# Kernel tuning notes

Measured on AMD Instinct MI355X. Metric: run time of the kernel, lower is better.

## Reference

```python
import jax, jax.numpy as jnp
import numpy as np

NX = NY = NZ = 64          # grid.shape
SPACING = 0.5              # Angstrom grid spacing
RESOLUTION = 2.0           # map resolution cutoff (A)
N_ATOMS = 128
K = 6                      # _range = 6 Gaussian terms (em=False)
CHUNK = 65536              # chunk_size over grid points


def setup_inputs() -> dict:
    key = jax.random.key(0)
    k1, k2, k3 = jax.random.split(key, 3)
    box = jnp.array([NX * SPACING, NY * SPACING, NZ * SPACING], jnp.float32)
    # atom coordinates uniform inside the box
    X = jax.random.uniform(k1, (N_ATOMS, 3), jnp.float32) * box
    # aw > 0, bw < 0 as produced by _setup_coeffs (aw = a*(-bw/pi)^1.5, bw = -pi^2/b)
    aw = jax.random.uniform(k2, (N_ATOMS, K), jnp.float32) * 4.0 + 0.5
    bw = -(jax.random.uniform(k3, (N_ATOMS, K), jnp.float32) * 4.0 + 0.5)
    # real-space grid, origin at 0 (center_shift folded in)
    xs = jnp.arange(NX, dtype=jnp.float32) * SPACING
    ys = jnp.arange(NY, dtype=jnp.float32) * SPACING
    zs = jnp.arange(NZ, dtype=jnp.float32) * SPACING
    gx, gy, gz = jnp.meshgrid(xs, ys, zs, indexing='ij')
    real_grid_flat = jnp.stack([gx, gy, gz], axis=-1).reshape(-1, 3)  # (G,3)
    # Fourier frequency magnitudes and radial Hamming filter (set_filter_and_mask)
    fx = jnp.fft.fftshift(jnp.fft.fftfreq(NX, SPACING)).astype(jnp.float32)
    fy = jnp.fft.fftshift(jnp.fft.fftfreq(NY, SPACING)).astype(jnp.float32)
    fz = jnp.fft.fftshift(jnp.fft.fftfreq(NZ, SPACING)).astype(jnp.float32)
    fxx, fyy, fzz = jnp.meshgrid(fx, fy, fz, indexing='ij')
    f_mag = jnp.sqrt(fxx ** 2 + fyy ** 2 + fzz ** 2)
    cutoff = 1.0 / RESOLUTION
    r_scaled = f_mag / cutoff
    hamming = jnp.where(f_mag <= cutoff,
                        0.54 + 0.46 * jnp.cos(jnp.pi * r_scaled),
                        0.0).astype(jnp.float32)
    return {"X": X, "aw": aw, "bw": bw,
            "real_grid_flat": real_grid_flat, "hamming": hamming}


def _density_flat(real_grid_flat, X, aw, bw):
    """Chunked sum-of-Gaussians splatting: density[g] = sum_a sum_k aw[a,k]*exp(bw[a,k]*|g-x_a|^2)."""
    def chunk_density(grid_chunk):  # (C,3)
        # squared distances grid-chunk x atoms, (C, A); cdist(...,p=2)**2 == sum of squared diffs
        d2 = jnp.sum((grid_chunk[:, None, :] - X[None, :, :]) ** 2, axis=-1)
        dens = jnp.zeros((grid_chunk.shape[0],), dtype=grid_chunk.dtype)
        for k in range(K):  # fixed small K=6, avoids (C,A,K) materialization
            dens = dens + jnp.sum(aw[None, :, k] * jnp.exp(bw[None, :, k] * d2), axis=-1)
        return dens
    G = real_grid_flat.shape[0]
    chunks = real_grid_flat.reshape(G // CHUNK, CHUNK, 3)
    dens = jax.lax.map(chunk_density, chunks)  # (n_chunks, CHUNK)
    return dens.reshape(G)


def _to_f_density(rho):
    ax = (-3, -2, -1)
    return jnp.fft.fftshift(
        jnp.fft.fftn(jnp.fft.ifftshift(rho, axes=ax), axes=ax, norm='ortho'), axes=ax)


def _to_density(f_map):
    ax = (-3, -2, -1)
    return jnp.fft.fftshift(
        jnp.fft.ifftn(jnp.fft.ifftshift(f_map, axes=ax), axes=ax, norm='ortho'), axes=ax)


def reference(X, aw, bw, real_grid_flat, hamming):
    rho = _density_flat(real_grid_flat, X, aw, bw).reshape(NX, NY, NZ)
    f_rho = _to_f_density(rho)
    f_filtered = f_rho * hamming            # radial Hamming low-pass at 1/resolution
    out = _to_density(f_filtered).real      # filtered real-space density
    # normalize() helper: zero mean, unit (population) std
    return (out - out.mean()) / (out.std() + 1e-8)
```

## Files before the change

kernel.cpp:

```cpp
#include <hip/hip_runtime.h>
#include <math.h>

#define NG (64*64*64)

typedef __bf16 v8bf __attribute__((ext_vector_type(8)));
typedef float  v4f  __attribute__((ext_vector_type(4)));

#define WS_W    0
#define WS_PART (2*1024*1024)

#define K_LIVE(k) ((k) <= 16 || (k) >= 48)

__device__ __forceinline__ float2 cadd(float2 a, float2 b) {
    return make_float2(a.x + b.x, a.y + b.y);
}
__device__ __forceinline__ float2 csub(float2 a, float2 b) {
    return make_float2(a.x - b.x, a.y - b.y);
}
template <bool CONJ>
__device__ __forceinline__ float2 mulmi(float2 a) {
    return CONJ ? make_float2(-a.y, a.x) : make_float2(a.y, -a.x);
}

template <bool CONJ>
__device__ __forceinline__ void fft8(const float2 x[8], float2 y[8])
{
    const float r = 0.70710678118654752f;
    float2 ee0 = cadd(x[0], x[4]), ee1 = csub(x[0], x[4]);
    float2 eo0 = cadd(x[2], x[6]), eo1 = csub(x[2], x[6]);
    float2 E0 = cadd(ee0, eo0), E2 = csub(ee0, eo0);
    float2 me = mulmi<CONJ>(eo1);
    float2 E1 = cadd(ee1, me), E3 = csub(ee1, me);
    float2 oe0 = cadd(x[1], x[5]), oe1 = csub(x[1], x[5]);
    float2 oo0 = cadd(x[3], x[7]), oo1 = csub(x[3], x[7]);
    float2 O0 = cadd(oe0, oo0), O2 = csub(oe0, oo0);
    float2 mo = mulmi<CONJ>(oo1);
    float2 O1 = cadd(oe1, mo), O3 = csub(oe1, mo);
    float2 W1O1 = CONJ ? make_float2(r * (O1.x - O1.y), r * (O1.x + O1.y))
                       : make_float2(r * (O1.x + O1.y), r * (O1.y - O1.x));
    float2 W2O2 = mulmi<CONJ>(O2);
    float2 W3O3 = CONJ ? make_float2(-r * (O3.x + O3.y), r * (O3.x - O3.y))
                       : make_float2(r * (O3.y - O3.x), -r * (O3.x + O3.y));
    y[0] = cadd(E0, O0);   y[4] = csub(E0, O0);
    y[1] = cadd(E1, W1O1); y[5] = csub(E1, W1O1);
    y[2] = cadd(E2, W2O2); y[6] = csub(E2, W2O2);
    y[3] = cadd(E3, W3O3); y[7] = csub(E3, W3O3);
}

template <bool CONJ>
__device__ __forceinline__ void xf64(const float2 xin[8], float2* L, int es,
                                     int t, const float2* tw, float2 y[8],
                                     bool active)
{
    float2 b[8];
    if (active) {
        fft8<CONJ>(xin, b);
#pragma unroll
        for (int k1 = 0; k1 < 8; ++k1) {
            float2 wv = tw[(t * k1) & 63];
            float ws = CONJ ? -wv.y : wv.y;
            float tr = b[k1].x * wv.x - b[k1].y * ws;
            float ti = b[k1].x * ws + b[k1].y * wv.x;
            b[k1] = make_float2(tr, ti);
        }
#pragma unroll
        for (int k1 = 0; k1 < 8; ++k1)
            L[(k1 * 8 + t) * es] = b[k1];
    }
    __syncthreads();
    if (active) {
        float2 a[8];
#pragma unroll
        for (int n1 = 0; n1 < 8; ++n1) a[n1] = L[(t * 8 + n1) * es];
        fft8<CONJ>(a, y);
    }
}

__device__ __forceinline__ void make_tw(float2* tw, int tid)
{
    if (tid < 64) {
        float ang = -6.28318530717958647692f * (float)tid / 64.0f;
        float s, c;
        sincosf(ang, &s, &c);
        tw[tid] = make_float2(c, s);
    }
}

__global__ __launch_bounds__(512) void density_fftz_kernel(
    const float* __restrict__ X, const float* __restrict__ aw,
    const float* __restrict__ bw, float2* __restrict__ W2)
{
    __shared__ __align__(16) __bf16 Ah[16][776];
    __shared__ __align__(16) __bf16 Al[16][776];
    __shared__ float2 D[16][66];
    __shared__ float2 tw[64];

    int tid = threadIdx.x;
    make_tw(tw, tid);

    int blk = blockIdx.x;
    int x  = blk >> 2;
    int yq = blk & 3;
    float px = 0.5f * (float)x;

    {
        int row = tid >> 5;
        int a0  = (tid & 31) * 4;
        float py = 0.5f * (float)(yq * 16 + row);
#pragma unroll
        for (int ai = 0; ai < 4; ++ai) {
            int a = a0 + ai;
            float dxa = px - X[3 * a + 0];
            float dya = py - X[3 * a + 1];
            float d2 = dxa * dxa + dya * dya;
            int jb = a * 6;
#pragma unroll
            for (int p = 0; p < 3; ++p) {
                int j = jb + 2 * p;
                float e0 = aw[j] * __expf(bw[j] * d2);
                float e1 = aw[j + 1] * __expf(bw[j + 1] * d2);
                __bf16 h0 = (__bf16)e0, h1 = (__bf16)e1;
                __bf16 l0 = (__bf16)(e0 - (float)h0);
                __bf16 l1 = (__bf16)(e1 - (float)h1);
                unsigned hp = ((unsigned)__builtin_bit_cast(unsigned short, h1) << 16)
                            | (unsigned)__builtin_bit_cast(unsigned short, h0);
                unsigned lp = ((unsigned)__builtin_bit_cast(unsigned short, l1) << 16)
                            | (unsigned)__builtin_bit_cast(unsigned short, l0);
                *(unsigned*)&Ah[row][j] = hp;
                *(unsigned*)&Al[row][j] = lp;
            }
        }
    }
    __syncthreads();

    {
        int w = tid >> 6;
        int l = tid & 63;
        int m = l & 15;
        int g = l >> 4;
        int zt = w & 3;
        int kh = w >> 2;
        float pz = 0.5f * (float)(zt * 16 + m);
        int jb0 = kh * 384 + g * 8;
        v4f accHH = {0.f, 0.f, 0.f, 0.f};
        v4f accHL = {0.f, 0.f, 0.f, 0.f};
        v4f accLH = {0.f, 0.f, 0.f, 0.f};
        const __bf16* ahp = &Ah[m][jb0];
        const __bf16* alp = &Al[m][jb0];
#pragma unroll 2
        for (int ks = 0; ks < 12; ++ks) {
            v8bf aH = *(const v8bf*)(ahp + ks * 32);
            v8bf aL = *(const v8bf*)(alp + ks * 32);
            v8bf bH, bL;
#pragma unroll
            for (int p = 0; p < 4; ++p) {
                int j = jb0 + ks * 32 + 2 * p;
                float2 bwp = *(const float2*)(bw + j);
                int a0 = j / 6, a1 = (j + 1) / 6;
                float dz0 = pz - X[3 * a0 + 2];
                float dz1 = pz - X[3 * a1 + 2];
                float e0 = __expf(bwp.x * dz0 * dz0);
                float e1 = __expf(bwp.y * dz1 * dz1);
                __bf16 h0 = (__bf16)e0, h1 = (__bf16)e1;
                bH[2 * p]     = h0;
                bH[2 * p + 1] = h1;
                bL[2 * p]     = (__bf16)(e0 - (float)h0);
                bL[2 * p + 1] = (__bf16)(e1 - (float)h1);
            }
            accHH = __builtin_amdgcn_mfma_f32_16x16x32_bf16(aH, bH, accHH, 0, 0, 0);
            accHL = __builtin_amdgcn_mfma_f32_16x16x32_bf16(aH, bL, accHL, 0, 0, 0);
            accLH = __builtin_amdgcn_mfma_f32_16x16x32_bf16(aL, bH, accLH, 0, 0, 0);
        }
#pragma unroll
        for (int r = 0; r < 4; ++r) {
            float s = accHH[r] + accHL[r] + accLH[r];
            if (kh == 0) D[g * 4 + r][zt * 16 + m].x = s;
            else         D[g * 4 + r][zt * 16 + m].y = s;
        }
    }
    __syncthreads();

    bool active = tid < 128;
    int lid = (tid >> 3) & 15, t = tid & 7;
    float2 xin[8], y[8];
    if (active) {
#pragma unroll
        for (int n2 = 0; n2 < 8; ++n2) {
            float2 v = D[lid][8 * n2 + t];
            xin[n2] = make_float2(v.x + v.y, 0.f);
        }
    }
    xf64<false>(xin, &D[lid][0], 1, t, tw, y, active);
    if (active) {
        int ybase = yq * 16 + lid;
#pragma unroll
        for (int k2 = 0; k2 < 8; ++k2) {
            int kz = t + 8 * k2;
            if (K_LIVE(kz))
                W2[kz * 4096 + x * 64 + ybase] = y[k2];
        }
    }
}

__global__ __launch_bounds__(512) void plane_kernel(
    float2* __restrict__ W2, const float* __restrict__ ham,
    double* __restrict__ partial)
{
    __shared__ float2 P[64][66];
    __shared__ float2 tw[64];
    __shared__ double red[8];
    int tid = threadIdx.x;
    make_tw(tw, tid);

    int z0 = blockIdx.x <= 16 ? blockIdx.x : blockIdx.x + 31;
    const float4* src = (const float4*)(W2 + z0 * 4096);
#pragma unroll
    for (int q = 0; q < 4; ++q) {
        int i = tid + q * 512;
        float4 v = src[i];
        int e = i * 2;
        P[e >> 6][e & 63] = make_float2(v.x, v.y);
        P[e >> 6][(e & 63) + 1] = make_float2(v.z, v.w);
    }
    __syncthreads();

    int lid = tid >> 3, t = tid & 7;
    float2 xin[8], y[8];

#pragma unroll
    for (int n2 = 0; n2 < 8; ++n2) xin[n2] = P[lid][8 * n2 + t];
    xf64<false>(xin, &P[lid][0], 1, t, tw, y, true);
    __syncthreads();
#pragma unroll
    for (int k2 = 0; k2 < 8; ++k2) P[lid][t + 8 * k2] = y[k2];
    __syncthreads();

    bool kyLive = K_LIVE(lid);
#pragma unroll
    for (int n2 = 0; n2 < 8; ++n2) xin[n2] = P[8 * n2 + t][lid];
    xf64<false>(xin, &P[0][lid], 66, t, tw, y, kyLive);
    if (kyLive) {
        int hyz = ((lid + 32) & 63) * 64 + ((z0 + 32) & 63);
#pragma unroll
        for (int k2 = 0; k2 < 8; ++k2) {
            int kx = t + 8 * k2;
            float h = ham[((kx + 32) & 63) * 4096 + hyz];
            y[k2].x *= h; y[k2].y *= h;
        }
    }
    {
        double s2 = 0.0;
        if (kyLive) {
#pragma unroll
            for (int k2 = 0; k2 < 8; ++k2)
                s2 += (double)y[k2].x * y[k2].x + (double)y[k2].y * y[k2].y;
        }
#pragma unroll
        for (int off = 32; off > 0; off >>= 1)
            s2 += __shfl_down(s2, off, 64);
        if ((tid & 63) == 0) red[tid >> 6] = s2;
        if (z0 == 0 && tid == 0)
            partial[64] = (double)y[0].x;
    }
    __syncthreads();
#pragma unroll
    for (int k2 = 0; k2 < 8; ++k2)
        P[t + 8 * k2][lid] = kyLive ? y[k2] : make_float2(0.f, 0.f);
    __syncthreads();
    if (tid == 0) {
        double s = 0.0;
#pragma unroll
        for (int i = 0; i < 8; ++i) s += red[i];
        partial[z0] = s;
    }

#pragma unroll
    for (int n2 = 0; n2 < 8; ++n2) xin[n2] = P[8 * n2 + t][lid];
    xf64<true>(xin, &P[0][lid], 66, t, tw, y, kyLive);
    __syncthreads();
    if (kyLive) {
#pragma unroll
        for (int k2 = 0; k2 < 8; ++k2) P[t + 8 * k2][lid] = y[k2];
    }
    __syncthreads();

#pragma unroll
    for (int n2 = 0; n2 < 8; ++n2) xin[n2] = P[lid][8 * n2 + t];
    xf64<true>(xin, &P[lid][0], 1, t, tw, y, true);
#pragma unroll
    for (int k2 = 0; k2 < 8; ++k2)
        W2[z0 * 4096 + lid * 64 + t + 8 * k2] = y[k2];
}

__global__ __launch_bounds__(128) void invz_norm_kernel(
    const float2* __restrict__ W2, const double* __restrict__ partial,
    float* __restrict__ outr)
{
    __shared__ float2 ln[16][66];
    __shared__ float2 tw[64];
    __shared__ float nrm[2];
    int tid = threadIdx.x;
    make_tw(tw, tid);
    if (tid < 64) {
        double s = K_LIVE(tid) ? partial[tid] : 0.0;
#pragma unroll
        for (int off = 32; off > 0; off >>= 1)
            s += __shfl_down(s, off, 64);
        if (tid == 0) {
            double mean = partial[64] * (1.0 / 262144.0);
            double var = s * (1.0 / 262144.0 / 262144.0) - mean * mean;
            nrm[0] = (float)mean;
            nrm[1] = (float)(1.0 / (sqrt(var > 0.0 ? var : 0.0) + 1e-8));
        }
    }
    __syncthreads();

    int lid = tid >> 3, t = tid & 7;
    int L = blockIdx.x * 16 + lid;
    float2 xin[8], y[8];
#pragma unroll
    for (int n2 = 0; n2 < 8; ++n2) {
        int kz = 8 * n2 + t;
        xin[n2] = K_LIVE(kz) ? W2[kz * 4096 + L] : make_float2(0.f, 0.f);
    }
    xf64<true>(xin, &ln[lid][0], 1, t, tw, y, true);

    float mean = nrm[0], rstd = nrm[1];
#pragma unroll
    for (int k2 = 0; k2 < 8; ++k2) {
        float v = y[k2].x * (1.0f / 262144.0f);
        outr[L * 64 + t + 8 * k2] = (v - mean) * rstd;
    }
}

extern "C" void kernel_launch(void* const* d_in, const int* in_sizes, int n_in,
                              void* d_out, int out_size, void* d_ws,
                              size_t ws_size, hipStream_t stream)
{
    const float* X   = (const float*)d_in[0];
    const float* aw  = (const float*)d_in[1];
    const float* bw  = (const float*)d_in[2];
    const float* ham = (const float*)d_in[4];
    float* out = (float*)d_out;

    char* ws = (char*)d_ws;
    float2* W2   = (float2*)(ws + WS_W);
    double* part = (double*)(ws + WS_PART);

    density_fftz_kernel<<<256, 512, 0, stream>>>(X, aw, bw, W2);
    plane_kernel<<<33, 512, 0, stream>>>(W2, ham, part);
    invz_norm_kernel<<<256, 128, 0, stream>>>(W2, part, out);
}
```

Measured before the change: 24.87 us.

## Exploit Hermitian symmetry in kz and fuse plane and inverse-z kernels

Because the density is real, its spectrum is Hermitian, so only kz 0..16 are computed and stored. The mirrored planes are rebuilt from their conjugates in the final inverse-z pass, and the energy sum is doubled for the non-zero planes. The plane kernel and the inverse-z/normalize kernel are merged into one launch: 17 producer blocks process the planes, and 64 consumer blocks spin on a global atomic counter before running the last pass. This removes one kernel launch and about half the plane work, but it relies on all producer blocks being scheduled alongside the spinning consumers, and it adds a spin-wait latency.

```diff
diff --git a/kernel.cpp b/kernel.cpp
--- a/kernel.cpp
+++ b/kernel.cpp
@@ -8,6 +8,7 @@
 
 #define WS_W    0
 #define WS_PART (2*1024*1024)
+#define WS_FLAG (WS_PART + 256)
 
 #define K_LIVE(k) ((k) <= 16 || (k) >= 48)
 
@@ -88,7 +89,8 @@
 
 __global__ __launch_bounds__(512) void density_fftz_kernel(
     const float* __restrict__ X, const float* __restrict__ aw,
-    const float* __restrict__ bw, float2* __restrict__ W2)
+    const float* __restrict__ bw, float2* __restrict__ W2,
+    int* __restrict__ flag)
 {
     __shared__ __align__(16) __bf16 Ah[16][776];
     __shared__ __align__(16) __bf16 Al[16][776];
@@ -97,6 +99,8 @@
 
     int tid = threadIdx.x;
     make_tw(tw, tid);
+    if (blockIdx.x == 0 && tid == 0)
+        __hip_atomic_store(flag, 0, __ATOMIC_RELAXED, __HIP_MEMORY_SCOPE_AGENT);
 
     int blk = blockIdx.x;
     int x  = blk >> 2;
@@ -196,140 +200,154 @@
 #pragma unroll
         for (int k2 = 0; k2 < 8; ++k2) {
             int kz = t + 8 * k2;
-            if (K_LIVE(kz))
+            if (kz <= 16)
                 W2[kz * 4096 + x * 64 + ybase] = y[k2];
         }
     }
 }
 
-__global__ __launch_bounds__(512) void plane_kernel(
+__global__ __launch_bounds__(512) void spectrum_inv_kernel(
     float2* __restrict__ W2, const float* __restrict__ ham,
-    double* __restrict__ partial)
+    double* __restrict__ partial, float* __restrict__ outr,
+    int* __restrict__ flag)
 {
     __shared__ float2 P[64][66];
     __shared__ float2 tw[64];
     __shared__ double red[8];
+    __shared__ float nrm[2];
+
     int tid = threadIdx.x;
+    int bid = blockIdx.x;
     make_tw(tw, tid);
 
-    int z0 = blockIdx.x <= 16 ? blockIdx.x : blockIdx.x + 31;
-    const float4* src = (const float4*)(W2 + z0 * 4096);
-#pragma unroll
-    for (int q = 0; q < 4; ++q) {
-        int i = tid + q * 512;
-        float4 v = src[i];
-        int e = i * 2;
-        P[e >> 6][e & 63] = make_float2(v.x, v.y);
-        P[e >> 6][(e & 63) + 1] = make_float2(v.z, v.w);
-    }
-    __syncthreads();
-
-    int lid = tid >> 3, t = tid & 7;
-    float2 xin[8], y[8];
-
-#pragma unroll
-    for (int n2 = 0; n2 < 8; ++n2) xin[n2] = P[lid][8 * n2 + t];
-    xf64<false>(xin, &P[lid][0], 1, t, tw, y, true);
-    __syncthreads();
-#pragma unroll
-    for (int k2 = 0; k2 < 8; ++k2) P[lid][t + 8 * k2] = y[k2];
-    __syncthreads();
-
-    bool kyLive = K_LIVE(lid);
-#pragma unroll
-    for (int n2 = 0; n2 < 8; ++n2) xin[n2] = P[8 * n2 + t][lid];
-    xf64<false>(xin, &P[0][lid], 66, t, tw, y, kyLive);
-    if (kyLive) {
-        int hyz = ((lid + 32) & 63) * 64 + ((z0 + 32) & 63);
+    if (bid < 17) {
+        int z0 = bid;
+        const float4* src = (const float4*)(W2 + z0 * 4096);
+#pragma unroll
+        for (int q = 0; q < 4; ++q) {
+            int i = tid + q * 512;
+            float4 v = src[i];
+            int e = i * 2;
+            P[e >> 6][e & 63] = make_float2(v.x, v.y);
+            P[e >> 6][(e & 63) + 1] = make_float2(v.z, v.w);
+        }
+        __syncthreads();
+
+        int lid = tid >> 3, t = tid & 7;
+        float2 xin[8], y[8];
+
+#pragma unroll
+        for (int n2 = 0; n2 < 8; ++n2) xin[n2] = P[lid][8 * n2 + t];
+        xf64<false>(xin, &P[lid][0], 1, t, tw, y, true);
+        __syncthreads();
+#pragma unroll
+        for (int k2 = 0; k2 < 8; ++k2) P[lid][t + 8 * k2] = y[k2];
+        __syncthreads();
+
+        bool kyLive = K_LIVE(lid);
+#pragma unroll
+        for (int n2 = 0; n2 < 8; ++n2) xin[n2] = P[8 * n2 + t][lid];
+        xf64<false>(xin, &P[0][lid], 66, t, tw, y, kyLive);
+        if (kyLive) {
+            int hyz = ((lid + 32) & 63) * 64 + ((z0 + 32) & 63);
+#pragma unroll
+            for (int k2 = 0; k2 < 8; ++k2) {
+                int kx = t + 8 * k2;
+                float h = ham[((kx + 32) & 63) * 4096 + hyz];
+                y[k2].x *= h; y[k2].y *= h;
+            }
+        }
+        {
+            double s2 = 0.0;
+            if (kyLive) {
+#pragma unroll
+                for (int k2 = 0; k2 < 8; ++k2)
+                    s2 += (double)y[k2].x * y[k2].x + (double)y[k2].y * y[k2].y;
+            }
+#pragma unroll
+            for (int off = 32; off > 0; off >>= 1)
+                s2 += __shfl_down(s2, off, 64);
+            if ((tid & 63) == 0) red[tid >> 6] = s2;
+            if (z0 == 0 && tid == 0)
+                partial[17] = (double)y[0].x;
+        }
+        __syncthreads();
+#pragma unroll
+        for (int k2 = 0; k2 < 8; ++k2)
+            P[t + 8 * k2][lid] = kyLive ? y[k2] : make_float2(0.f, 0.f);
+        __syncthreads();
+        if (tid == 0) {
+            double s = 0.0;
+#pragma unroll
+            for (int i = 0; i < 8; ++i) s += red[i];
+            partial[z0] = (z0 == 0 ? 1.0 : 2.0) * s;
+        }
+
+#pragma unroll
+        for (int n2 = 0; n2 < 8; ++n2) xin[n2] = P[8 * n2 + t][lid];
+        xf64<true>(xin, &P[0][lid], 66, t, tw, y, kyLive);
+        __syncthreads();
+        if (kyLive) {
+#pragma unroll
+            for (int k2 = 0; k2 < 8; ++k2) P[t + 8 * k2][lid] = y[k2];
+        }
+        __syncthreads();
+
+#pragma unroll
+        for (int n2 = 0; n2 < 8; ++n2) xin[n2] = P[lid][8 * n2 + t];
+        xf64<true>(xin, &P[lid][0], 1, t, tw, y, true);
+#pragma unroll
+        for (int k2 = 0; k2 < 8; ++k2)
+            W2[z0 * 4096 + lid * 64 + t + 8 * k2] = y[k2];
+
+        __syncthreads();
+        if (tid == 0)
+            __hip_atomic_fetch_add(flag, 1, __ATOMIC_ACQ_REL,
+                                   __HIP_MEMORY_SCOPE_AGENT);
+    } else {
+        if (tid == 0) {
+            while (__hip_atomic_load(flag, __ATOMIC_ACQUIRE,
+                                     __HIP_MEMORY_SCOPE_AGENT) < 17)
+                __builtin_amdgcn_s_sleep(8);
+        }
+        __syncthreads();
+
+        if (tid < 64) {
+            double s = (tid <= 16) ? partial[tid] : 0.0;
+#pragma unroll
+            for (int off = 32; off > 0; off >>= 1)
+                s += __shfl_down(s, off, 64);
+            if (tid == 0) {
+                double mean = partial[17] * (1.0 / 262144.0);
+                double var = s * (1.0 / 262144.0 / 262144.0) - mean * mean;
+                nrm[0] = (float)mean;
+                nrm[1] = (float)(1.0 / (sqrt(var > 0.0 ? var : 0.0) + 1e-8));
+            }
+        }
+
+        int lid = tid >> 3, t = tid & 7;
+        int L = (bid - 17) * 64 + lid;
+        float2 xin[8], y[8];
+#pragma unroll
+        for (int n2 = 0; n2 < 8; ++n2) {
+            int kz = 8 * n2 + t;
+            if (kz <= 16) {
+                xin[n2] = W2[kz * 4096 + L];
+            } else if (kz >= 48) {
+                float2 v = W2[(64 - kz) * 4096 + L];
+                xin[n2] = make_float2(v.x, -v.y);
+            } else {
+                xin[n2] = make_float2(0.f, 0.f);
+            }
+        }
+        xf64<true>(xin, &P[lid][0], 1, t, tw, y, true);
+
+        float mean = nrm[0], rstd = nrm[1];
 #pragma unroll
         for (int k2 = 0; k2 < 8; ++k2) {
-            int kx = t + 8 * k2;
-            float h = ham[((kx + 32) & 63) * 4096 + hyz];
-            y[k2].x *= h; y[k2].y *= h;
-        }
-    }
-    {
-        double s2 = 0.0;
-        if (kyLive) {
-#pragma unroll
-            for (int k2 = 0; k2 < 8; ++k2)
-                s2 += (double)y[k2].x * y[k2].x + (double)y[k2].y * y[k2].y;
-        }
-#pragma unroll
-        for (int off = 32; off > 0; off >>= 1)
-            s2 += __shfl_down(s2, off, 64);
-        if ((tid & 63) == 0) red[tid >> 6] = s2;
-        if (z0 == 0 && tid == 0)
-            partial[64] = (double)y[0].x;
-    }
-    __syncthreads();
-#pragma unroll
-    for (int k2 = 0; k2 < 8; ++k2)
-        P[t + 8 * k2][lid] = kyLive ? y[k2] : make_float2(0.f, 0.f);
-    __syncthreads();
-    if (tid == 0) {
-        double s = 0.0;
-#pragma unroll
-        for (int i = 0; i < 8; ++i) s += red[i];
-        partial[z0] = s;
-    }
-
-#pragma unroll
-    for (int n2 = 0; n2 < 8; ++n2) xin[n2] = P[8 * n2 + t][lid];
-    xf64<true>(xin, &P[0][lid], 66, t, tw, y, kyLive);
-    __syncthreads();
-    if (kyLive) {
-#pragma unroll
-        for (int k2 = 0; k2 < 8; ++k2) P[t + 8 * k2][lid] = y[k2];
-    }
-    __syncthreads();
-
-#pragma unroll
-    for (int n2 = 0; n2 < 8; ++n2) xin[n2] = P[lid][8 * n2 + t];
-    xf64<true>(xin, &P[lid][0], 1, t, tw, y, true);
-#pragma unroll
-    for (int k2 = 0; k2 < 8; ++k2)
-        W2[z0 * 4096 + lid * 64 + t + 8 * k2] = y[k2];
-}
-
-__global__ __launch_bounds__(128) void invz_norm_kernel(
-    const float2* __restrict__ W2, const double* __restrict__ partial,
-    float* __restrict__ outr)
-{
-    __shared__ float2 ln[16][66];
-    __shared__ float2 tw[64];
-    __shared__ float nrm[2];
-    int tid = threadIdx.x;
-    make_tw(tw, tid);
-    if (tid < 64) {
-        double s = K_LIVE(tid) ? partial[tid] : 0.0;
-#pragma unroll
-        for (int off = 32; off > 0; off >>= 1)
-            s += __shfl_down(s, off, 64);
-        if (tid == 0) {
-            double mean = partial[64] * (1.0 / 262144.0);
-            double var = s * (1.0 / 262144.0 / 262144.0) - mean * mean;
-            nrm[0] = (float)mean;
-            nrm[1] = (float)(1.0 / (sqrt(var > 0.0 ? var : 0.0) + 1e-8));
-        }
-    }
-    __syncthreads();
-
-    int lid = tid >> 3, t = tid & 7;
-    int L = blockIdx.x * 16 + lid;
-    float2 xin[8], y[8];
-#pragma unroll
-    for (int n2 = 0; n2 < 8; ++n2) {
-        int kz = 8 * n2 + t;
-        xin[n2] = K_LIVE(kz) ? W2[kz * 4096 + L] : make_float2(0.f, 0.f);
-    }
-    xf64<true>(xin, &ln[lid][0], 1, t, tw, y, true);
-
-    float mean = nrm[0], rstd = nrm[1];
-#pragma unroll
-    for (int k2 = 0; k2 < 8; ++k2) {
-        float v = y[k2].x * (1.0f / 262144.0f);
-        outr[L * 64 + t + 8 * k2] = (v - mean) * rstd;
+            float v = y[k2].x * (1.0f / 262144.0f);
+            outr[L * 64 + t + 8 * k2] = (v - mean) * rstd;
+        }
     }
 }
 
@@ -346,8 +364,8 @@
     char* ws = (char*)d_ws;
     float2* W2   = (float2*)(ws + WS_W);
     double* part = (double*)(ws + WS_PART);
-
-    density_fftz_kernel<<<256, 512, 0, stream>>>(X, aw, bw, W2);
-    plane_kernel<<<33, 512, 0, stream>>>(W2, ham, part);
-    invz_norm_kernel<<<256, 128, 0, stream>>>(W2, part, out);
-}
+    int*    flag = (int*)(ws + WS_FLAG);
+
+    density_fftz_kernel<<<256, 512, 0, stream>>>(X, aw, bw, W2, flag);
+    spectrum_inv_kernel<<<81, 512, 0, stream>>>(W2, ham, part, out, flag);
+}
```

New measurement: 30.47 us. 1.23x slower.
